# Kernel optimization log

Hardware: AMD Instinct MI355X
Metric: run time of the kernel (lower is better)

Reference implementation:

```python
import jax, jax.numpy as jnp
import numpy as np
from jax import lax

B, S, D = 2, 4096, 1024
E, H, K = 8, 2816, 2  # hidden_dim 4096 -> int(2*4096/3)=2730 -> round up to multiple_of 256 -> 2816


def setup_inputs() -> dict:
    key = jax.random.key(0)
    ks = jax.random.split(key, 5)
    scale = 0.02
    return {
        "x": jax.random.normal(ks[0], (B, S, D), dtype=jnp.float32),
        "router_w": jax.random.normal(ks[1], (E, D), dtype=jnp.float32) * scale,
        "w1": jax.random.normal(ks[2], (E, D, H), dtype=jnp.float32) * scale,
        "w2": jax.random.normal(ks[3], (E, H, D), dtype=jnp.float32) * scale,
        "w3": jax.random.normal(ks[4], (E, D, H), dtype=jnp.float32) * scale,
        "top_k": K,
    }


def reference(x, router_w, w1, w2, w3, top_k):
    b, s, d = x.shape
    e = router_w.shape[0]
    xf = x.reshape(-1, d)                                # [T, D]
    logits = xf @ router_w.T                             # [T, E]
    vals, idx = lax.top_k(logits, top_k)                 # [T, K]
    rw = jax.nn.softmax(vals.astype(jnp.float32), axis=-1).astype(x.dtype)  # [T, K]
    # combine[t, e] = routing weight of expert e for token t (0 if not selected)
    combine = jnp.sum(jax.nn.one_hot(idx, e, dtype=x.dtype) * rw[..., None], axis=1)  # [T, E]

    def body(acc, ew):
        w1e, w2e, w3e, ce = ew                           # [D,H], [H,D], [D,H], [T]
        h = jax.nn.silu(xf @ w1e) * (xf @ w3e)           # SwiGLU FFN, [T, H]
        return acc + (h @ w2e) * ce[:, None], None

    out, _ = lax.scan(body, jnp.zeros_like(xf), (w1, w2, w3, combine.T))
    return out.reshape(b, s, d)
```

## Files before the change

### kernel.cpp

```cpp
#include <hip/hip_runtime.h>
#include <stdint.h>

#define T_TOK 8192
#define DIM   1024
#define NE    8
#define NH    2816
#define NROWS (T_TOK*2)

typedef __attribute__((ext_vector_type(8))) __bf16 bf16x8;
typedef __attribute__((ext_vector_type(4))) float  f32x4;

typedef __attribute__((address_space(1))) const unsigned int g_as1;
typedef __attribute__((address_space(3))) unsigned int l_as3;
#define GLL(g, l) __builtin_amdgcn_global_load_lds((g_as1*)(g), (l_as3*)(l), 16, 0, 0)

__device__ __forceinline__ unsigned short f2bf(float f){
  union { float f; uint32_t u; } v; v.f = f;
  uint32_t r = (v.u + 0x7FFFu + ((v.u >> 16) & 1u)) >> 16;
  return (unsigned short)r;
}


__global__ void init_k(int* counts, int* cursor){
  int i = threadIdx.x;
  if (i < NE){ counts[i] = 0; cursor[i] = 0; }
}

__global__ void zero_out_k(float4* __restrict__ out){
  int i = blockIdx.x*blockDim.x + threadIdx.x;
  const int n4 = T_TOK*DIM/4;
  const float4 z = make_float4(0.f,0.f,0.f,0.f);
  for (; i < n4; i += gridDim.x*blockDim.x) out[i] = z;
}

__global__ void cvt_k(const float* __restrict__ x, unsigned short* __restrict__ xbf){
  int i = blockIdx.x*blockDim.x + threadIdx.x;
  const int total = T_TOK*DIM/8;
  for (; i < total; i += gridDim.x*blockDim.x){
    const float4 a = *(const float4*)(x + (size_t)i*8);
    const float4 b = *(const float4*)(x + (size_t)i*8 + 4);
    ushort4 lo = make_ushort4(f2bf(a.x), f2bf(a.y), f2bf(a.z), f2bf(a.w));
    ushort4 hi = make_ushort4(f2bf(b.x), f2bf(b.y), f2bf(b.z), f2bf(b.w));
    *(ushort4*)(xbf + (size_t)i*8)     = lo;
    *(ushort4*)(xbf + (size_t)i*8 + 4) = hi;
  }
}

__global__ __launch_bounds__(256) void transp_k(const float* __restrict__ in,
    unsigned short* __restrict__ outp, int R, int C)
{
  __shared__ unsigned short Tl[64*68];
  const int r0 = blockIdx.x*64, c0 = blockIdx.y*64;
  const size_t mbase = (size_t)blockIdx.z * (size_t)R * (size_t)C;
  const float* ip = in + mbase;
  unsigned short* op = outp + mbase;
  const int t = threadIdx.x;
  #pragma unroll
  for (int i=0;i<4;i++){
    const int r  = (t>>4) + i*16;
    const int cq = t & 15;
    const float4 v = *(const float4*)(ip + (size_t)(r0+r)*C + c0 + cq*4);
    Tl[(cq*4+0)*68 + r] = f2bf(v.x);
    Tl[(cq*4+1)*68 + r] = f2bf(v.y);
    Tl[(cq*4+2)*68 + r] = f2bf(v.z);
    Tl[(cq*4+3)*68 + r] = f2bf(v.w);
  }
  __syncthreads();
  #pragma unroll
  for (int i=0;i<4;i++){
    const int idx = i*1024 + t*4;
    const int c = idx>>6, r = idx&63;
    const ushort4 v = *(const ushort4*)&Tl[c*68 + r];
    *(ushort4*)(op + (size_t)(c0+c)*R + r0 + r) = v;
  }
}

__global__ __launch_bounds__(256) void transp2_k(const float* __restrict__ w1,
    const float* __restrict__ w3, unsigned short* __restrict__ w1t,
    unsigned short* __restrict__ w3t)
{
  __shared__ unsigned short Tl[64*68];
  const int r0 = blockIdx.x*64, c0 = blockIdx.y*64;
  const int z = blockIdx.z;
  const size_t mbase = (size_t)(z & (NE-1)) * (size_t)DIM * (size_t)NH;
  const float* ip = (z < NE ? w1 : w3) + mbase;
  unsigned short* op = (z < NE ? w1t : w3t) + mbase;
  const int t = threadIdx.x;
  #pragma unroll
  for (int i=0;i<4;i++){
    const int r  = (t>>4) + i*16;
    const int cq = t & 15;
    const float4 v = *(const float4*)(ip + (size_t)(r0+r)*NH + c0 + cq*4);
    Tl[(cq*4+0)*68 + r] = f2bf(v.x);
    Tl[(cq*4+1)*68 + r] = f2bf(v.y);
    Tl[(cq*4+2)*68 + r] = f2bf(v.z);
    Tl[(cq*4+3)*68 + r] = f2bf(v.w);
  }
  __syncthreads();
  #pragma unroll
  for (int i=0;i<4;i++){
    const int idx = i*1024 + t*4;
    const int c = idx>>6, r = idx&63;
    const ushort4 v = *(const ushort4*)&Tl[c*68 + r];
    *(ushort4*)(op + (size_t)(c0+c)*DIM + r0 + r) = v;
  }
}


__global__ void router_k(const float* __restrict__ x, const float* __restrict__ rw,
                         int* __restrict__ topk_e, float* __restrict__ topk_w,
                         int* __restrict__ counts){
  const int t = blockIdx.x;
  const int l = threadIdx.x;
  const float* xr = x + (size_t)t * DIM;
  float acc[NE];
  #pragma unroll
  for (int e=0;e<NE;e++) acc[e] = 0.f;
  #pragma unroll
  for (int i=0;i<DIM/64;i++){
    float xv = xr[l + 64*i];
    #pragma unroll
    for (int e=0;e<NE;e++) acc[e] += xv * rw[e*DIM + l + 64*i];
  }
  #pragma unroll
  for (int e=0;e<NE;e++){
    float v = acc[e];
    #pragma unroll
    for (int off=32; off; off>>=1) v += __shfl_xor(v, off);
    acc[e] = v;
  }
  if (l == 0){
    int e0 = 0; float v0 = acc[0];
    #pragma unroll
    for (int e=1;e<NE;e++) if (acc[e] > v0){ v0 = acc[e]; e0 = e; }
    int e1 = -1; float v1 = -1e30f;
    #pragma unroll
    for (int e=0;e<NE;e++) if (e != e0 && acc[e] > v1){ v1 = acc[e]; e1 = e; }
    float ex = __expf(v1 - v0);
    float s  = 1.f + ex;
    topk_e[t*2]   = e0;  topk_e[t*2+1] = e1;
    topk_w[t*2]   = 1.f/s; topk_w[t*2+1] = ex/s;
    atomicAdd(&counts[e0], 1);
    atomicAdd(&counts[e1], 1);
  }
}

__global__ void prefix_k(const int* __restrict__ counts, int* __restrict__ offs){
  if (threadIdx.x == 0 && blockIdx.x == 0){
    int s = 0;
    for (int e=0;e<NE;e++){ offs[e] = s; s += counts[e]; }
  }
}

__global__ void scatter_k(const int* __restrict__ topk_e, const float* __restrict__ topk_w,
                          const int* __restrict__ offs, int* __restrict__ cursor,
                          int* __restrict__ row_tok, float* __restrict__ row_w){
  int t = blockIdx.x*blockDim.x + threadIdx.x;
  if (t >= T_TOK) return;
  #pragma unroll
  for (int k=0;k<2;k++){
    int e = topk_e[t*2+k];
    int p = atomicAdd(&cursor[e], 1);
    int flat = offs[e] + p;
    row_tok[flat] = t;
    row_w[flat]   = topk_w[t*2+k];
  }
}


__global__ __launch_bounds__(512,2) void gemm1_bf(
    const unsigned short* __restrict__ xbf,
    const unsigned short* __restrict__ w1t, const unsigned short* __restrict__ w3t,
    unsigned short* __restrict__ hbuf,
    const int* __restrict__ row_tok,
    const int* __restrict__ counts, const int* __restrict__ offs)
{
  __shared__ unsigned short Al [2][128*32];
  __shared__ unsigned short B1l[2][128*32];
  __shared__ unsigned short B3l[2][128*32];

  const int i   = blockIdx.y*64 + blockIdx.x;
  const int lid = (i & 7)*1408 + (i >> 3);
  const int e   = lid / 1408;
  const int rem = lid - e*1408;
  const int h0  = (rem >> 6) * 128;
  const int rb  = rem & 63;

  const int cnt = counts[e];
  const int row0 = rb * 128;
  if (row0 >= cnt) return;
  const int nv   = min(128, cnt - row0);
  const int base = offs[e] + row0;

  const int t  = threadIdx.x;
  const int srow = t >> 2, sch = t & 3;
  const int tok = row_tok[base + min(srow, nv-1)];
  const unsigned short* asrc = xbf + (size_t)tok*DIM + sch*8;
  const unsigned short* b1s  = w1t + ((size_t)(e*NH + h0 + srow))*DIM + sch*8;
  const unsigned short* b3s  = w3t + ((size_t)(e*NH + h0 + srow))*DIM + sch*8;
  const int lo = t*16;

  const int wid = t >> 6, l = t & 63;
  const int wr = wid >> 2, wc = wid & 3;
  const int lr = l & 15,  lk = l >> 4;

  f32x4 acc1[4][2], acc3[4][2];
  #pragma unroll
  for (int m=0;m<4;m++)
    #pragma unroll
    for (int n=0;n<2;n++){ acc1[m][n] = (f32x4)0.f; acc3[m][n] = (f32x4)0.f; }

  GLL(asrc, (char*)Al [0] + lo);
  GLL(b1s,  (char*)B1l[0] + lo);
  GLL(b3s,  (char*)B3l[0] + lo);
  __syncthreads();

  for (int kk=0; kk<DIM/32; ++kk){
    const int cur = kk & 1;
    if (kk < DIM/32 - 1){
      const int k1 = (kk+1)*32;
      GLL(asrc + k1, (char*)Al [cur^1] + lo);
      GLL(b1s  + k1, (char*)B1l[cur^1] + lo);
      GLL(b3s  + k1, (char*)B3l[cur^1] + lo);
    }
    bf16x8 a[4], b1[2], b3[2];
    #pragma unroll
    for (int m=0;m<4;m++) a[m] = *(const bf16x8*)&Al[cur][(wr*64 + m*16 + lr)*32 + lk*8];
    #pragma unroll
    for (int n=0;n<2;n++){
      b1[n] = *(const bf16x8*)&B1l[cur][(wc*32 + n*16 + lr)*32 + lk*8];
      b3[n] = *(const bf16x8*)&B3l[cur][(wc*32 + n*16 + lr)*32 + lk*8];
    }
    #pragma unroll
    for (int m=0;m<4;m++)
      #pragma unroll
      for (int n=0;n<2;n++){
        acc1[m][n] = __builtin_amdgcn_mfma_f32_16x16x32_bf16(a[m], b1[n], acc1[m][n], 0,0,0);
        acc3[m][n] = __builtin_amdgcn_mfma_f32_16x16x32_bf16(a[m], b3[n], acc3[m][n], 0,0,0);
      }
    __syncthreads();
  }

  #pragma unroll
  for (int m=0;m<4;m++){
    #pragma unroll
    for (int i2=0;i2<4;i2++){
      const int r = wr*64 + m*16 + lk*4 + i2;
      if (r < nv){
        const size_t rowbase = (size_t)(base + r) * NH;
        #pragma unroll
        for (int n=0;n<2;n++){
          float z  = acc1[m][n][i2];
          float p3 = acc3[m][n][i2];
          float hv = (z / (1.f + __expf(-z))) * p3;
          hbuf[rowbase + h0 + wc*32 + n*16 + lr] = f2bf(hv);
        }
      }
    }
  }
}

__global__ __launch_bounds__(512,2) void gemm2_bf(
    const unsigned short* __restrict__ hbuf,
    const unsigned short* __restrict__ w2t,
    float* __restrict__ out,
    const int* __restrict__ row_tok, const float* __restrict__ row_w,
    const int* __restrict__ counts, const int* __restrict__ offs)
{
  __shared__ unsigned short Al[2][128*32];
  __shared__ unsigned short Bl[2][128*32];

  const int i   = blockIdx.y*64 + blockIdx.x;
  const int lid = (i & 7)*512 + (i >> 3);
  const int e   = lid >> 9;
  const int rem = lid & 511;
  const int d0  = (rem >> 6) * 128;
  const int rb  = rem & 63;

  const int cnt = counts[e];
  const int row0 = rb * 128;
  if (row0 >= cnt) return;
  const int nv   = min(128, cnt - row0);
  const int base = offs[e] + row0;

  const int t  = threadIdx.x;
  const int srow = t >> 2, sch = t & 3;
  const unsigned short* asrc = hbuf + (size_t)(base + min(srow, nv-1))*NH + sch*8;
  const unsigned short* bs   = w2t + ((size_t)(e*DIM + d0 + srow))*NH + sch*8;
  const int lo = t*16;

  const int wid = t >> 6, l = t & 63;
  const int wr = wid >> 2, wc = wid & 3;
  const int lr = l & 15,  lk = l >> 4;

  f32x4 acc[4][2];
  #pragma unroll
  for (int m=0;m<4;m++)
    #pragma unroll
    for (int n=0;n<2;n++) acc[m][n] = (f32x4)0.f;

  GLL(asrc, (char*)Al[0] + lo);
  GLL(bs,   (char*)Bl[0] + lo);
  __syncthreads();

  for (int kk=0; kk<NH/32; ++kk){
    const int cur = kk & 1;
    if (kk < NH/32 - 1){
      const int k1 = (kk+1)*32;
      GLL(asrc + k1, (char*)Al[cur^1] + lo);
      GLL(bs   + k1, (char*)Bl[cur^1] + lo);
    }
    bf16x8 a[4], b[2];
    #pragma unroll
    for (int m=0;m<4;m++) a[m] = *(const bf16x8*)&Al[cur][(wr*64 + m*16 + lr)*32 + lk*8];
    #pragma unroll
    for (int n=0;n<2;n++)  b[n] = *(const bf16x8*)&Bl[cur][(wc*32 + n*16 + lr)*32 + lk*8];
    #pragma unroll
    for (int m=0;m<4;m++)
      #pragma unroll
      for (int n=0;n<2;n++)
        acc[m][n] = __builtin_amdgcn_mfma_f32_16x16x32_bf16(a[m], b[n], acc[m][n], 0,0,0);
    __syncthreads();
  }

  #pragma unroll
  for (int m=0;m<4;m++){
    #pragma unroll
    for (int i2=0;i2<4;i2++){
      const int r = wr*64 + m*16 + lk*4 + i2;
      if (r < nv){
        const int flat = base + r;
        const int tok  = row_tok[flat];
        const float wgt = row_w[flat];
        float* orow = out + (size_t)tok * DIM + d0 + wc*32;
        #pragma unroll
        for (int n=0;n<2;n++)
          atomicAdd(&orow[n*16 + lr], acc[m][n][i2] * wgt);
      }
    }
  }
}


__global__ __launch_bounds__(256) void gemm1_k(
    const unsigned short* __restrict__ xbf,
    const float* __restrict__ w1, const float* __restrict__ w3,
    unsigned short* __restrict__ hbuf,
    const int* __restrict__ row_tok,
    const int* __restrict__ counts, const int* __restrict__ offs)
{
  __shared__ unsigned short Al [128*32];
  __shared__ unsigned short B1l[128*32];
  __shared__ unsigned short B3l[128*32];
  const int e   = blockIdx.y >> 6;
  const int rb  = blockIdx.y & 63;
  const int cnt = counts[e];
  const int row0 = rb * 128;
  if (row0 >= cnt) return;
  const int nv   = min(128, cnt - row0);
  const int base = offs[e] + row0;
  const int h0   = blockIdx.x * 128;
  const int t  = threadIdx.x;
  const int ar0 = t >> 2;
  const int ac  = t & 3;
  const int tok0 = row_tok[base + min(ar0,      nv-1)];
  const int tok1 = row_tok[base + min(ar0 + 64, nv-1)];
  const size_t asrc0 = (size_t)tok0 * DIM + ac*8;
  const size_t asrc1 = (size_t)tok1 * DIM + ac*8;
  const int dg = t >> 5;
  const int hq = t & 31;
  const float* w1p = w1 + (size_t)e * DIM * NH + (size_t)(h0 + hq*4);
  const float* w3p = w3 + (size_t)e * DIM * NH + (size_t)(h0 + hq*4);
  const int wid = t >> 6, l = t & 63;
  const int wr = wid >> 1, wc = wid & 1;
  const int lr = l & 15,  lk = l >> 4;
  f32x4 acc1[4][4], acc3[4][4];
  #pragma unroll
  for (int m=0;m<4;m++)
    #pragma unroll
    for (int n=0;n<4;n++){ acc1[m][n] = (f32x4)0.f; acc3[m][n] = (f32x4)0.f; }
  for (int kk=0; kk<DIM/32; ++kk){
    const int k0 = kk*32;
    __syncthreads();
    *(uint4*)&Al[ar0*32 + ac*8]      = *(const uint4*)(xbf + asrc0 + k0);
    *(uint4*)&Al[(ar0+64)*32 + ac*8] = *(const uint4*)(xbf + asrc1 + k0);
    {
      const float4 f0 = *(const float4*)(w1p + (size_t)(k0 + dg*4 + 0)*NH);
      const float4 f1 = *(const float4*)(w1p + (size_t)(k0 + dg*4 + 1)*NH);
      const float4 f2 = *(const float4*)(w1p + (size_t)(k0 + dg*4 + 2)*NH);
      const float4 f3 = *(const float4*)(w1p + (size_t)(k0 + dg*4 + 3)*NH);
      const float* p0=(const float*)&f0; const float* p1=(const float*)&f1;
      const float* p2=(const float*)&f2; const float* p3=(const float*)&f3;
      #pragma unroll
      for (int j=0;j<4;j++){
        ushort4 pk = make_ushort4(f2bf(p0[j]), f2bf(p1[j]), f2bf(p2[j]), f2bf(p3[j]));
        *(ushort4*)&B1l[(hq*4+j)*32 + dg*4] = pk;
      }
      const float4 g0 = *(const float4*)(w3p + (size_t)(k0 + dg*4 + 0)*NH);
      const float4 g1 = *(const float4*)(w3p + (size_t)(k0 + dg*4 + 1)*NH);
      const float4 g2 = *(const float4*)(w3p + (size_t)(k0 + dg*4 + 2)*NH);
      const float4 g3 = *(const float4*)(w3p + (size_t)(k0 + dg*4 + 3)*NH);
      const float* q0=(const float*)&g0; const float* q1=(const float*)&g1;
      const float* q2=(const float*)&g2; const float* q3=(const float*)&g3;
      #pragma unroll
      for (int j=0;j<4;j++){
        ushort4 pk = make_ushort4(f2bf(q0[j]), f2bf(q1[j]), f2bf(q2[j]), f2bf(q3[j]));
        *(ushort4*)&B3l[(hq*4+j)*32 + dg*4] = pk;
      }
    }
    __syncthreads();
    bf16x8 a[4], b1[4], b3[4];
    #pragma unroll
    for (int m=0;m<4;m++) a[m] = *(const bf16x8*)&Al[(wr*64 + m*16 + lr)*32 + lk*8];
    #pragma unroll
    for (int n=0;n<4;n++){
      b1[n] = *(const bf16x8*)&B1l[(wc*64 + n*16 + lr)*32 + lk*8];
      b3[n] = *(const bf16x8*)&B3l[(wc*64 + n*16 + lr)*32 + lk*8];
    }
    #pragma unroll
    for (int m=0;m<4;m++)
      #pragma unroll
      for (int n=0;n<4;n++){
        acc1[m][n] = __builtin_amdgcn_mfma_f32_16x16x32_bf16(a[m], b1[n], acc1[m][n], 0,0,0);
        acc3[m][n] = __builtin_amdgcn_mfma_f32_16x16x32_bf16(a[m], b3[n], acc3[m][n], 0,0,0);
      }
  }
  #pragma unroll
  for (int m=0;m<4;m++){
    #pragma unroll
    for (int i=0;i<4;i++){
      const int r = wr*64 + m*16 + lk*4 + i;
      if (r < nv){
        const size_t rowbase = (size_t)(base + r) * NH;
        #pragma unroll
        for (int n=0;n<4;n++){
          float z  = acc1[m][n][i];
          float p3 = acc3[m][n][i];
          float hv = (z / (1.f + __expf(-z))) * p3;
          hbuf[rowbase + h0 + wc*64 + n*16 + lr] = f2bf(hv);
        }
      }
    }
  }
}

__global__ __launch_bounds__(256) void gemm2_k(
    const unsigned short* __restrict__ hbuf,
    const float* __restrict__ w2,
    float* __restrict__ out,
    const int* __restrict__ row_tok, const float* __restrict__ row_w,
    const int* __restrict__ counts, const int* __restrict__ offs)
{
  __shared__ unsigned short Al[128*32];
  __shared__ unsigned short Bl[128*32];
  const int e   = blockIdx.y >> 6;
  const int rb  = blockIdx.y & 63;
  const int cnt = counts[e];
  const int row0 = rb * 128;
  if (row0 >= cnt) return;
  const int nv   = min(128, cnt - row0);
  const int base = offs[e] + row0;
  const int d0   = blockIdx.x * 128;
  const int t  = threadIdx.x;
  const int ar0 = t >> 2;
  const int ac  = t & 3;
  const size_t asrc0 = (size_t)(base + min(ar0,      nv-1)) * NH + ac*8;
  const size_t asrc1 = (size_t)(base + min(ar0 + 64, nv-1)) * NH + ac*8;
  const int dg = t >> 5;
  const int hq = t & 31;
  const float* w2p = w2 + (size_t)e * NH * DIM + (size_t)(d0 + hq*4);
  const int wid = t >> 6, l = t & 63;
  const int wr = wid >> 1, wc = wid & 1;
  const int lr = l & 15,  lk = l >> 4;
  f32x4 acc[4][4];
  #pragma unroll
  for (int m=0;m<4;m++)
    #pragma unroll
    for (int n=0;n<4;n++) acc[m][n] = (f32x4)0.f;
  for (int kk=0; kk<NH/32; ++kk){
    const int k0 = kk*32;
    __syncthreads();
    *(uint4*)&Al[ar0*32 + ac*8]      = *(const uint4*)(hbuf + asrc0 + k0);
    *(uint4*)&Al[(ar0+64)*32 + ac*8] = *(const uint4*)(hbuf + asrc1 + k0);
    {
      const float4 f0 = *(const float4*)(w2p + (size_t)(k0 + dg*4 + 0)*DIM);
      const float4 f1 = *(const float4*)(w2p + (size_t)(k0 + dg*4 + 1)*DIM);
      const float4 f2 = *(const float4*)(w2p + (size_t)(k0 + dg*4 + 2)*DIM);
      const float4 f3 = *(const float4*)(w2p + (size_t)(k0 + dg*4 + 3)*DIM);
      const float* p0=(const float*)&f0; const float* p1=(const float*)&f1;
      const float* p2=(const float*)&f2; const float* p3=(const float*)&f3;
      #pragma unroll
      for (int j=0;j<4;j++){
        ushort4 pk = make_ushort4(f2bf(p0[j]), f2bf(p1[j]), f2bf(p2[j]), f2bf(p3[j]));
        *(ushort4*)&Bl[(hq*4+j)*32 + dg*4] = pk;
      }
    }
    __syncthreads();
    bf16x8 a[4], b[4];
    #pragma unroll
    for (int m=0;m<4;m++) a[m] = *(const bf16x8*)&Al[(wr*64 + m*16 + lr)*32 + lk*8];
    #pragma unroll
    for (int n=0;n<4;n++)  b[n] = *(const bf16x8*)&Bl[(wc*64 + n*16 + lr)*32 + lk*8];
    #pragma unroll
    for (int m=0;m<4;m++)
      #pragma unroll
      for (int n=0;n<4;n++)
        acc[m][n] = __builtin_amdgcn_mfma_f32_16x16x32_bf16(a[m], b[n], acc[m][n], 0,0,0);
  }
  #pragma unroll
  for (int m=0;m<4;m++){
    #pragma unroll
    for (int i=0;i<4;i++){
      const int r = wr*64 + m*16 + lk*4 + i;
      if (r < nv){
        const int flat = base + r;
        const int tok  = row_tok[flat];
        const float wgt = row_w[flat];
        float* orow = out + (size_t)tok * DIM + d0 + wc*64;
        #pragma unroll
        for (int n=0;n<4;n++)
          atomicAdd(&orow[n*16 + lr], acc[m][n][i] * wgt);
      }
    }
  }
}


extern "C" void kernel_launch(void* const* d_in, const int* in_sizes, int n_in,
                              void* d_out, int out_size, void* d_ws, size_t ws_size,
                              hipStream_t stream) {
  (void)in_sizes; (void)n_in; (void)out_size;
  const float* x   = (const float*)d_in[0];
  const float* rw  = (const float*)d_in[1];
  const float* w1  = (const float*)d_in[2];
  const float* w2  = (const float*)d_in[3];
  const float* w3  = (const float*)d_in[4];
  float* out = (float*)d_out;
  char* ws = (char*)d_ws;

  const size_t SZ_XBF  = (size_t)T_TOK*DIM*2;
  const size_t SZ_HBUF = (size_t)NROWS*NH*2;
  const size_t SZ_WT   = (size_t)NE*NH*DIM*2;
  const size_t SZ_SMALL = (size_t)NROWS*4*2 + (size_t)T_TOK*2*4*2 + 3*64*4 + 4096;
  const size_t NEED_FAST = SZ_XBF + SZ_HBUF + 2*SZ_WT + SZ_SMALL;

  if (ws_size >= NEED_FAST) {
    size_t off = 0;
    unsigned short* xbf  = (unsigned short*)(ws + off); off += SZ_XBF;
    unsigned short* hbuf = (unsigned short*)(ws + off); off += SZ_HBUF;
    unsigned short* w1t  = (unsigned short*)(ws + off); off += SZ_WT;
    unsigned short* w3t  = (unsigned short*)(ws + off); off += SZ_WT;
    unsigned short* w2t  = w1t;
    int*   row_tok = (int*)  (ws + off); off += NROWS*4;
    float* row_w   = (float*)(ws + off); off += NROWS*4;
    int*   topk_e  = (int*)  (ws + off); off += T_TOK*2*4;
    float* topk_w  = (float*)(ws + off); off += T_TOK*2*4;
    int*   counts  = (int*)  (ws + off); off += 64;
    int*   offs    = (int*)  (ws + off); off += 64;
    int*   cursor  = (int*)  (ws + off); off += 64;

    init_k    <<<1, 64, 0, stream>>>(counts, cursor);
    zero_out_k<<<2048, 256, 0, stream>>>((float4*)out);
    cvt_k     <<<2048, 256, 0, stream>>>(x, xbf);
    router_k  <<<T_TOK, 64, 0, stream>>>(x, rw, topk_e, topk_w, counts);
    prefix_k  <<<1, 64, 0, stream>>>(counts, offs);
    scatter_k <<<(T_TOK+255)/256, 256, 0, stream>>>(topk_e, topk_w, offs, cursor, row_tok, row_w);
    transp2_k <<<dim3(DIM/64, NH/64, 2*NE), 256, 0, stream>>>(w1, w3, w1t, w3t);
    gemm1_bf  <<<dim3(64, NE*22), 512, 0, stream>>>(xbf, w1t, w3t, hbuf, row_tok, counts, offs);
    transp_k  <<<dim3(NH/64, DIM/64, NE), 256, 0, stream>>>(w2, w2t, NH, DIM);
    gemm2_bf  <<<dim3(64, NE*8), 512, 0, stream>>>(hbuf, w2t, out, row_tok, row_w, counts, offs);
  } else {
    size_t off = 0;
    unsigned short* xbf  = (unsigned short*)(ws + off); off += SZ_XBF;
    unsigned short* hbuf = (unsigned short*)(ws + off); off += SZ_HBUF;
    int*   row_tok = (int*)  (ws + off); off += NROWS*4;
    float* row_w   = (float*)(ws + off); off += NROWS*4;
    int*   topk_e  = (int*)  (ws + off); off += T_TOK*2*4;
    float* topk_w  = (float*)(ws + off); off += T_TOK*2*4;
    int*   counts  = (int*)  (ws + off); off += 64;
    int*   offs    = (int*)  (ws + off); off += 64;
    int*   cursor  = (int*)  (ws + off); off += 64;

    init_k    <<<1, 64, 0, stream>>>(counts, cursor);
    zero_out_k<<<2048, 256, 0, stream>>>((float4*)out);
    cvt_k     <<<2048, 256, 0, stream>>>(x, xbf);
    router_k  <<<T_TOK, 64, 0, stream>>>(x, rw, topk_e, topk_w, counts);
    prefix_k  <<<1, 64, 0, stream>>>(counts, offs);
    scatter_k <<<(T_TOK+255)/256, 256, 0, stream>>>(topk_e, topk_w, offs, cursor, row_tok, row_w);
    gemm1_k   <<<dim3(NH/128, NE*64), 256, 0, stream>>>(xbf, w1, w3, hbuf, row_tok, counts, offs);
    gemm2_k   <<<dim3(DIM/128, NE*64), 256, 0, stream>>>(hbuf, w2, out, row_tok, row_w, counts, offs);
  }
}
```

Before: 770.8 us.

## Triple-buffer expert GEMM LDS pipeline with XOR swizzle and single barrier

Both expert GEMM kernels move from a double-buffered LDS scheme with two __syncthreads per k-step to a three-stage ring. Loads are issued two tiles ahead, and each step waits on an explicit vmcnt before a single s_barrier. Global-to-LDS chunk placement and the matching fragment reads are XOR-swizzled by row to cut LDS bank conflicts. s_setprio is raised around the MFMA block. This should hide more global-load latency and reduce stalls, at the cost of more LDS per block (72KB for gemm1), which could limit occupancy.

```diff
diff --git a/kernel.cpp b/kernel.cpp
--- a/kernel.cpp
+++ b/kernel.cpp
@@ -168,16 +168,16 @@
 }
 
 
-__global__ __launch_bounds__(512,2) void gemm1_bf(
+__global__ __launch_bounds__(512,2) void gemm1_p(
     const unsigned short* __restrict__ xbf,
     const unsigned short* __restrict__ w1t, const unsigned short* __restrict__ w3t,
     unsigned short* __restrict__ hbuf,
     const int* __restrict__ row_tok,
     const int* __restrict__ counts, const int* __restrict__ offs)
 {
-  __shared__ unsigned short Al [2][128*32];
-  __shared__ unsigned short B1l[2][128*32];
-  __shared__ unsigned short B3l[2][128*32];
+  __shared__ unsigned short As [3][128*32];
+  __shared__ unsigned short B1s[3][128*32];
+  __shared__ unsigned short B3s[3][128*32];
 
   const int i   = blockIdx.y*64 + blockIdx.x;
   const int lid = (i & 7)*1408 + (i >> 3);
@@ -191,18 +191,21 @@
   if (row0 >= cnt) return;
   const int nv   = min(128, cnt - row0);
   const int base = offs[e] + row0;
-
-  const int t  = threadIdx.x;
-  const int srow = t >> 2, sch = t & 3;
-  const int tok = row_tok[base + min(srow, nv-1)];
-  const unsigned short* asrc = xbf + (size_t)tok*DIM + sch*8;
-  const unsigned short* b1s  = w1t + ((size_t)(e*NH + h0 + srow))*DIM + sch*8;
-  const unsigned short* b3s  = w3t + ((size_t)(e*NH + h0 + srow))*DIM + sch*8;
+  const int NK   = DIM/32;
+
+  const int t = threadIdx.x;
+  const int r_loc = t >> 2, sct = t & 3;
+  const int csw = (sct ^ ((r_loc >> 1) & 3)) * 8;
+  const int tok = row_tok[base + min(r_loc, nv-1)];
+  const unsigned short* aS  = xbf + (size_t)tok*DIM + csw;
+  const unsigned short* b1S = w1t + ((size_t)(e*NH + h0) + r_loc)*DIM + csw;
+  const unsigned short* b3S = w3t + ((size_t)(e*NH + h0) + r_loc)*DIM + csw;
   const int lo = t*16;
 
   const int wid = t >> 6, l = t & 63;
   const int wr = wid >> 2, wc = wid & 3;
   const int lr = l & 15,  lk = l >> 4;
+  const int rc = (lk ^ ((lr >> 1) & 3)) * 8;
 
   f32x4 acc1[4][2], acc3[4][2];
   #pragma unroll
@@ -210,27 +213,35 @@
     #pragma unroll
     for (int n=0;n<2;n++){ acc1[m][n] = (f32x4)0.f; acc3[m][n] = (f32x4)0.f; }
 
-  GLL(asrc, (char*)Al [0] + lo);
-  GLL(b1s,  (char*)B1l[0] + lo);
-  GLL(b3s,  (char*)B3l[0] + lo);
-  __syncthreads();
-
-  for (int kk=0; kk<DIM/32; ++kk){
-    const int cur = kk & 1;
-    if (kk < DIM/32 - 1){
-      const int k1 = (kk+1)*32;
-      GLL(asrc + k1, (char*)Al [cur^1] + lo);
-      GLL(b1s  + k1, (char*)B1l[cur^1] + lo);
-      GLL(b3s  + k1, (char*)B3l[cur^1] + lo);
-    }
+  GLL(aS,      (char*)As[0]+lo); GLL(b1S,      (char*)B1s[0]+lo); GLL(b3S,      (char*)B3s[0]+lo);
+  GLL(aS+32,   (char*)As[1]+lo); GLL(b1S+32,   (char*)B1s[1]+lo); GLL(b3S+32,   (char*)B3s[1]+lo);
+
+  for (int kt=0; kt<NK; ++kt){
+    if (kt < NK-1) asm volatile("s_waitcnt vmcnt(3)" ::: "memory");
+    else           asm volatile("s_waitcnt vmcnt(0)" ::: "memory");
+    __builtin_amdgcn_s_barrier();
+
+    if (kt+2 < NK){
+      const int kA = (kt+2)*32;
+      char* ad  = (char*)As [(kt+2)%3];
+      char* b1d = (char*)B1s[(kt+2)%3];
+      char* b3d = (char*)B3s[(kt+2)%3];
+      GLL(aS+kA, ad+lo); GLL(b1S+kA, b1d+lo); GLL(b3S+kA, b3d+lo);
+    }
+
+    const unsigned short* Ab  = As [kt%3];
+    const unsigned short* B1b = B1s[kt%3];
+    const unsigned short* B3b = B3s[kt%3];
+
     bf16x8 a[4], b1[2], b3[2];
     #pragma unroll
-    for (int m=0;m<4;m++) a[m] = *(const bf16x8*)&Al[cur][(wr*64 + m*16 + lr)*32 + lk*8];
+    for (int m=0;m<4;m++) a[m] = *(const bf16x8*)&Ab[(wr*64 + m*16 + lr)*32 + rc];
     #pragma unroll
     for (int n=0;n<2;n++){
-      b1[n] = *(const bf16x8*)&B1l[cur][(wc*32 + n*16 + lr)*32 + lk*8];
-      b3[n] = *(const bf16x8*)&B3l[cur][(wc*32 + n*16 + lr)*32 + lk*8];
-    }
+      b1[n] = *(const bf16x8*)&B1b[(wc*32 + n*16 + lr)*32 + rc];
+      b3[n] = *(const bf16x8*)&B3b[(wc*32 + n*16 + lr)*32 + rc];
+    }
+    __builtin_amdgcn_s_setprio(1);
     #pragma unroll
     for (int m=0;m<4;m++)
       #pragma unroll
@@ -238,7 +249,7 @@
         acc1[m][n] = __builtin_amdgcn_mfma_f32_16x16x32_bf16(a[m], b1[n], acc1[m][n], 0,0,0);
         acc3[m][n] = __builtin_amdgcn_mfma_f32_16x16x32_bf16(a[m], b3[n], acc3[m][n], 0,0,0);
       }
-    __syncthreads();
+    __builtin_amdgcn_s_setprio(0);
   }
 
   #pragma unroll
@@ -260,15 +271,15 @@
   }
 }
 
-__global__ __launch_bounds__(512,2) void gemm2_bf(
+__global__ __launch_bounds__(512,2) void gemm2_p(
     const unsigned short* __restrict__ hbuf,
     const unsigned short* __restrict__ w2t,
     float* __restrict__ out,
     const int* __restrict__ row_tok, const float* __restrict__ row_w,
     const int* __restrict__ counts, const int* __restrict__ offs)
 {
-  __shared__ unsigned short Al[2][128*32];
-  __shared__ unsigned short Bl[2][128*32];
+  __shared__ unsigned short As[3][128*32];
+  __shared__ unsigned short Bs[3][128*32];
 
   const int i   = blockIdx.y*64 + blockIdx.x;
   const int lid = (i & 7)*512 + (i >> 3);
@@ -282,16 +293,19 @@
   if (row0 >= cnt) return;
   const int nv   = min(128, cnt - row0);
   const int base = offs[e] + row0;
-
-  const int t  = threadIdx.x;
-  const int srow = t >> 2, sch = t & 3;
-  const unsigned short* asrc = hbuf + (size_t)(base + min(srow, nv-1))*NH + sch*8;
-  const unsigned short* bs   = w2t + ((size_t)(e*DIM + d0 + srow))*NH + sch*8;
+  const int NK   = NH/32;
+
+  const int t = threadIdx.x;
+  const int r_loc = t >> 2, sct = t & 3;
+  const int csw = (sct ^ ((r_loc >> 1) & 3)) * 8;
+  const unsigned short* aS = hbuf + (size_t)(base + min(r_loc, nv-1))*NH + csw;
+  const unsigned short* bS = w2t + ((size_t)(e*DIM + d0) + r_loc)*NH + csw;
   const int lo = t*16;
 
   const int wid = t >> 6, l = t & 63;
   const int wr = wid >> 2, wc = wid & 3;
   const int lr = l & 15,  lk = l >> 4;
+  const int rc = (lk ^ ((lr >> 1) & 3)) * 8;
 
   f32x4 acc[4][2];
   #pragma unroll
@@ -299,28 +313,36 @@
     #pragma unroll
     for (int n=0;n<2;n++) acc[m][n] = (f32x4)0.f;
 
-  GLL(asrc, (char*)Al[0] + lo);
-  GLL(bs,   (char*)Bl[0] + lo);
-  __syncthreads();
-
-  for (int kk=0; kk<NH/32; ++kk){
-    const int cur = kk & 1;
-    if (kk < NH/32 - 1){
-      const int k1 = (kk+1)*32;
-      GLL(asrc + k1, (char*)Al[cur^1] + lo);
-      GLL(bs   + k1, (char*)Bl[cur^1] + lo);
-    }
+  GLL(aS,    (char*)As[0]+lo); GLL(bS,    (char*)Bs[0]+lo);
+  GLL(aS+32, (char*)As[1]+lo); GLL(bS+32, (char*)Bs[1]+lo);
+
+  for (int kt=0; kt<NK; ++kt){
+    if (kt < NK-1) asm volatile("s_waitcnt vmcnt(2)" ::: "memory");
+    else           asm volatile("s_waitcnt vmcnt(0)" ::: "memory");
+    __builtin_amdgcn_s_barrier();
+
+    if (kt+2 < NK){
+      const int kA = (kt+2)*32;
+      char* ad = (char*)As[(kt+2)%3];
+      char* bd = (char*)Bs[(kt+2)%3];
+      GLL(aS+kA, ad+lo); GLL(bS+kA, bd+lo);
+    }
+
+    const unsigned short* Ab = As[kt%3];
+    const unsigned short* Bb = Bs[kt%3];
+
     bf16x8 a[4], b[2];
     #pragma unroll
-    for (int m=0;m<4;m++) a[m] = *(const bf16x8*)&Al[cur][(wr*64 + m*16 + lr)*32 + lk*8];
-    #pragma unroll
-    for (int n=0;n<2;n++)  b[n] = *(const bf16x8*)&Bl[cur][(wc*32 + n*16 + lr)*32 + lk*8];
+    for (int m=0;m<4;m++) a[m] = *(const bf16x8*)&Ab[(wr*64 + m*16 + lr)*32 + rc];
+    #pragma unroll
+    for (int n=0;n<2;n++)  b[n] = *(const bf16x8*)&Bb[(wc*32 + n*16 + lr)*32 + rc];
+    __builtin_amdgcn_s_setprio(1);
     #pragma unroll
     for (int m=0;m<4;m++)
       #pragma unroll
       for (int n=0;n<2;n++)
         acc[m][n] = __builtin_amdgcn_mfma_f32_16x16x32_bf16(a[m], b[n], acc[m][n], 0,0,0);
-    __syncthreads();
+    __builtin_amdgcn_s_setprio(0);
   }
 
   #pragma unroll
@@ -566,9 +588,9 @@
     prefix_k  <<<1, 64, 0, stream>>>(counts, offs);
     scatter_k <<<(T_TOK+255)/256, 256, 0, stream>>>(topk_e, topk_w, offs, cursor, row_tok, row_w);
     transp2_k <<<dim3(DIM/64, NH/64, 2*NE), 256, 0, stream>>>(w1, w3, w1t, w3t);
-    gemm1_bf  <<<dim3(64, NE*22), 512, 0, stream>>>(xbf, w1t, w3t, hbuf, row_tok, counts, offs);
+    gemm1_p   <<<dim3(64, NE*22), 512, 0, stream>>>(xbf, w1t, w3t, hbuf, row_tok, counts, offs);
     transp_k  <<<dim3(NH/64, DIM/64, NE), 256, 0, stream>>>(w2, w2t, NH, DIM);
-    gemm2_bf  <<<dim3(64, NE*8), 512, 0, stream>>>(hbuf, w2t, out, row_tok, row_w, counts, offs);
+    gemm2_p   <<<dim3(64, NE*8), 512, 0, stream>>>(hbuf, w2t, out, row_tok, row_w, counts, offs);
   } else {
     size_t off = 0;
     unsigned short* xbf  = (unsigned short*)(ws + off); off += SZ_XBF;
```

After: 755.9 us. About the same (-1.9%).

## Enlarge MoE GEMM tiles to 256 rows with swizzled LDS and phased pipeline

Applied to the files above, without the earlier changes.

Both expert GEMMs now use 256-row token tiles with K-steps of 64, and gemm2 also widens to 256 output columns. LDS uses an XOR swizzle to avoid bank conflicts, and the next tile's global-to-LDS loads are split across four compute phases with explicit vmcnt waits, barriers and setprio around MFMA bursts. The aim is more data reuse per loaded byte and better overlap of loads with matrix math. In exchange, register and LDS use rise and there are fewer blocks, which can hurt occupancy and tail balance across experts with uneven token counts.

```diff
diff --git a/kernel.cpp b/kernel.cpp
--- a/kernel.cpp
+++ b/kernel.cpp
@@ -13,6 +13,7 @@
 typedef __attribute__((address_space(1))) const unsigned int g_as1;
 typedef __attribute__((address_space(3))) unsigned int l_as3;
 #define GLL(g, l) __builtin_amdgcn_global_load_lds((g_as1*)(g), (l_as3*)(l), 16, 0, 0)
+#define MFMA16(a,b,c) __builtin_amdgcn_mfma_f32_16x16x32_bf16(a,b,c,0,0,0)
 
 __device__ __forceinline__ unsigned short f2bf(float f){
   union { float f; uint32_t u; } v; v.f = f;
@@ -168,16 +169,16 @@
 }
 
 
-__global__ __launch_bounds__(512,2) void gemm1_bf(
+__global__ __launch_bounds__(512,2) void gemm1_8p(
     const unsigned short* __restrict__ xbf,
     const unsigned short* __restrict__ w1t, const unsigned short* __restrict__ w3t,
     unsigned short* __restrict__ hbuf,
     const int* __restrict__ row_tok,
     const int* __restrict__ counts, const int* __restrict__ offs)
 {
-  __shared__ unsigned short Al [2][128*32];
-  __shared__ unsigned short B1l[2][128*32];
-  __shared__ unsigned short B3l[2][128*32];
+  __shared__ unsigned short As [2][256*64];
+  __shared__ unsigned short B1s[2][128*64];
+  __shared__ unsigned short B3s[2][128*64];
 
   const int i   = blockIdx.y*64 + blockIdx.x;
   const int lid = (i & 7)*1408 + (i >> 3);
@@ -186,66 +187,115 @@
   const int h0  = (rem >> 6) * 128;
   const int rb  = rem & 63;
 
-  const int cnt = counts[e];
-  const int row0 = rb * 128;
+  const int cnt  = counts[e];
+  const int row0 = rb * 256;
   if (row0 >= cnt) return;
-  const int nv   = min(128, cnt - row0);
+  const int nv   = min(256, cnt - row0);
   const int base = offs[e] + row0;
+  const int NK   = DIM/64;
 
   const int t  = threadIdx.x;
-  const int srow = t >> 2, sch = t & 3;
-  const int tok = row_tok[base + min(srow, nv-1)];
-  const unsigned short* asrc = xbf + (size_t)tok*DIM + sch*8;
-  const unsigned short* b1s  = w1t + ((size_t)(e*NH + h0 + srow))*DIM + sch*8;
-  const unsigned short* b3s  = w3t + ((size_t)(e*NH + h0 + srow))*DIM + sch*8;
+  const int r8 = t >> 3, sl = t & 7;
+  const int csw = ((sl ^ (r8 & 7)) << 3);
+  const int tk0 = row_tok[base + min(r8,       nv-1)];
+  const int tk1 = row_tok[base + min(r8 + 64,  nv-1)];
+  const int tk2 = row_tok[base + min(r8 + 128, nv-1)];
+  const int tk3 = row_tok[base + min(r8 + 192, nv-1)];
+  const unsigned short* aP0 = xbf + (size_t)tk0*DIM + csw;
+  const unsigned short* aP1 = xbf + (size_t)tk1*DIM + csw;
+  const unsigned short* aP2 = xbf + (size_t)tk2*DIM + csw;
+  const unsigned short* aP3 = xbf + (size_t)tk3*DIM + csw;
+  const unsigned short* b1P0 = w1t + ((size_t)(e*NH + h0) + r8)*DIM + csw;
+  const unsigned short* b1P1 = b1P0 + (size_t)64*DIM;
+  const unsigned short* b3P0 = w3t + ((size_t)(e*NH + h0) + r8)*DIM + csw;
+  const unsigned short* b3P1 = b3P0 + (size_t)64*DIM;
   const int lo = t*16;
 
   const int wid = t >> 6, l = t & 63;
   const int wr = wid >> 2, wc = wid & 3;
   const int lr = l & 15,  lk = l >> 4;
 
-  f32x4 acc1[4][2], acc3[4][2];
-  #pragma unroll
-  for (int m=0;m<4;m++)
+  f32x4 acc1[8][2], acc3[8][2];
+  #pragma unroll
+  for (int m=0;m<8;m++)
     #pragma unroll
     for (int n=0;n<2;n++){ acc1[m][n] = (f32x4)0.f; acc3[m][n] = (f32x4)0.f; }
 
-  GLL(asrc, (char*)Al [0] + lo);
-  GLL(b1s,  (char*)B1l[0] + lo);
-  GLL(b3s,  (char*)B3l[0] + lo);
-  __syncthreads();
-
-  for (int kk=0; kk<DIM/32; ++kk){
-    const int cur = kk & 1;
-    if (kk < DIM/32 - 1){
-      const int k1 = (kk+1)*32;
-      GLL(asrc + k1, (char*)Al [cur^1] + lo);
-      GLL(b1s  + k1, (char*)B1l[cur^1] + lo);
-      GLL(b3s  + k1, (char*)B3l[cur^1] + lo);
-    }
-    bf16x8 a[4], b1[2], b3[2];
-    #pragma unroll
-    for (int m=0;m<4;m++) a[m] = *(const bf16x8*)&Al[cur][(wr*64 + m*16 + lr)*32 + lk*8];
-    #pragma unroll
-    for (int n=0;n<2;n++){
-      b1[n] = *(const bf16x8*)&B1l[cur][(wc*32 + n*16 + lr)*32 + lk*8];
-      b3[n] = *(const bf16x8*)&B3l[cur][(wc*32 + n*16 + lr)*32 + lk*8];
-    }
-    #pragma unroll
-    for (int m=0;m<4;m++)
-      #pragma unroll
-      for (int n=0;n<2;n++){
-        acc1[m][n] = __builtin_amdgcn_mfma_f32_16x16x32_bf16(a[m], b1[n], acc1[m][n], 0,0,0);
-        acc3[m][n] = __builtin_amdgcn_mfma_f32_16x16x32_bf16(a[m], b3[n], acc3[m][n], 0,0,0);
-      }
-    __syncthreads();
-  }
-
-  #pragma unroll
-  for (int m=0;m<4;m++){
+  GLL(b1P0, (char*)B1s[0] + lo);          GLL(b1P1, (char*)B1s[0] + 8192 + lo);
+  GLL(b3P0, (char*)B3s[0] + lo);          GLL(b3P1, (char*)B3s[0] + 8192 + lo);
+  GLL(aP0,  (char*)As[0]  + lo);          GLL(aP2,  (char*)As[0]  + 16384 + lo);
+  GLL(aP1,  (char*)As[0]  + 8192 + lo);   GLL(aP3,  (char*)As[0]  + 24576 + lo);
+  asm volatile("s_waitcnt vmcnt(2)" ::: "memory");
+  __builtin_amdgcn_s_barrier();
+
+  for (int kt=0; kt<NK; ++kt){
+    const int cur = kt & 1;
+    const int kof = (kt+1)*64;
+    const unsigned short* Ab  = As [cur];
+    const unsigned short* B1b = B1s[cur];
+    const unsigned short* B3b = B3s[cur];
+    char* Ad  = (char*)As [cur^1];
+    char* B1d = (char*)B1s[cur^1];
+    char* B3d = (char*)B3s[cur^1];
+    const bool st = (kt+1 < NK);
+
+    bf16x8 b1f[2][2], b3f[2][2];
+    #pragma unroll
+    for (int p=0; p<4; ++p){
+      bf16x8 a[2][2];
+      #pragma unroll
+      for (int j=0;j<2;j++){
+        const int row = wr*128 + (p*2+j)*16 + lr;
+        #pragma unroll
+        for (int ks=0;ks<2;ks++){
+          const int ck = ks*4 + lk;
+          a[j][ks] = *(const bf16x8*)&Ab[row*64 + ((ck ^ (row & 7)) << 3)];
+        }
+      }
+      if (p==0){
+        #pragma unroll
+        for (int n=0;n<2;n++){
+          const int brow = wc*32 + n*16 + lr;
+          #pragma unroll
+          for (int ks=0;ks<2;ks++){
+            const int ck = ks*4 + lk;
+            const int boff = brow*64 + ((ck ^ (brow & 7)) << 3);
+            b1f[n][ks] = *(const bf16x8*)&B1b[boff];
+            b3f[n][ks] = *(const bf16x8*)&B3b[boff];
+          }
+        }
+      }
+      if (st){
+        if      (p==0){ GLL(b1P0+kof, B1d+lo);      GLL(b1P1+kof, B1d+8192+lo); }
+        else if (p==1){ GLL(b3P0+kof, B3d+lo);      GLL(b3P1+kof, B3d+8192+lo); }
+        else if (p==2){ GLL(aP0+kof,  Ad+lo);       GLL(aP2+kof,  Ad+16384+lo); }
+        else          { GLL(aP1+kof,  Ad+8192+lo);  GLL(aP3+kof,  Ad+24576+lo); }
+      }
+      if (p==1){ if (st) asm volatile("s_waitcnt vmcnt(4)" ::: "memory");
+                 else    asm volatile("s_waitcnt vmcnt(0)" ::: "memory"); }
+      if (p==3){ asm volatile("s_waitcnt vmcnt(2)" ::: "memory"); }
+      __builtin_amdgcn_s_barrier();
+      asm volatile("s_waitcnt lgkmcnt(0)" ::: "memory");
+      __builtin_amdgcn_s_setprio(1);
+      #pragma unroll
+      for (int j=0;j<2;j++)
+        #pragma unroll
+        for (int ks=0;ks<2;ks++)
+          #pragma unroll
+          for (int n=0;n<2;n++){
+            acc1[p*2+j][n] = MFMA16(a[j][ks], b1f[n][ks], acc1[p*2+j][n]);
+            acc3[p*2+j][n] = MFMA16(a[j][ks], b3f[n][ks], acc3[p*2+j][n]);
+          }
+      __builtin_amdgcn_s_setprio(0);
+      __builtin_amdgcn_s_barrier();
+    }
+  }
+
+  #pragma unroll
+  for (int m=0;m<8;m++){
     #pragma unroll
     for (int i2=0;i2<4;i2++){
-      const int r = wr*64 + m*16 + lk*4 + i2;
+      const int r = wr*128 + m*16 + lk*4 + i2;
       if (r < nv){
         const size_t rowbase = (size_t)(base + r) * NH;
         #pragma unroll
@@ -260,81 +310,129 @@
   }
 }
 
-__global__ __launch_bounds__(512,2) void gemm2_bf(
+__global__ __launch_bounds__(512,2) void gemm2_8p(
     const unsigned short* __restrict__ hbuf,
     const unsigned short* __restrict__ w2t,
     float* __restrict__ out,
     const int* __restrict__ row_tok, const float* __restrict__ row_w,
     const int* __restrict__ counts, const int* __restrict__ offs)
 {
-  __shared__ unsigned short Al[2][128*32];
-  __shared__ unsigned short Bl[2][128*32];
+  __shared__ unsigned short As[2][256*64];
+  __shared__ unsigned short Bs[2][256*64];
 
   const int i   = blockIdx.y*64 + blockIdx.x;
-  const int lid = (i & 7)*512 + (i >> 3);
-  const int e   = lid >> 9;
-  const int rem = lid & 511;
-  const int d0  = (rem >> 6) * 128;
+  const int lid = (i & 7)*256 + (i >> 3);
+  const int e   = lid >> 8;
+  const int rem = lid & 255;
+  const int d0  = (rem >> 6) * 256;
   const int rb  = rem & 63;
 
-  const int cnt = counts[e];
-  const int row0 = rb * 128;
+  const int cnt  = counts[e];
+  const int row0 = rb * 256;
   if (row0 >= cnt) return;
-  const int nv   = min(128, cnt - row0);
+  const int nv   = min(256, cnt - row0);
   const int base = offs[e] + row0;
+  const int NK   = NH/64;
 
   const int t  = threadIdx.x;
-  const int srow = t >> 2, sch = t & 3;
-  const unsigned short* asrc = hbuf + (size_t)(base + min(srow, nv-1))*NH + sch*8;
-  const unsigned short* bs   = w2t + ((size_t)(e*DIM + d0 + srow))*NH + sch*8;
+  const int r8 = t >> 3, sl = t & 7;
+  const int csw = ((sl ^ (r8 & 7)) << 3);
+  const unsigned short* aP0 = hbuf + (size_t)(base + min(r8,       nv-1))*NH + csw;
+  const unsigned short* aP1 = hbuf + (size_t)(base + min(r8 + 64,  nv-1))*NH + csw;
+  const unsigned short* aP2 = hbuf + (size_t)(base + min(r8 + 128, nv-1))*NH + csw;
+  const unsigned short* aP3 = hbuf + (size_t)(base + min(r8 + 192, nv-1))*NH + csw;
+  const unsigned short* bP0 = w2t + ((size_t)(e*DIM + d0) + r8)*NH + csw;
+  const unsigned short* bP1 = bP0 + (size_t)64*NH;
+  const unsigned short* bP2 = bP0 + (size_t)128*NH;
+  const unsigned short* bP3 = bP0 + (size_t)192*NH;
   const int lo = t*16;
 
   const int wid = t >> 6, l = t & 63;
   const int wr = wid >> 2, wc = wid & 3;
   const int lr = l & 15,  lk = l >> 4;
 
-  f32x4 acc[4][2];
-  #pragma unroll
-  for (int m=0;m<4;m++)
-    #pragma unroll
-    for (int n=0;n<2;n++) acc[m][n] = (f32x4)0.f;
-
-  GLL(asrc, (char*)Al[0] + lo);
-  GLL(bs,   (char*)Bl[0] + lo);
-  __syncthreads();
-
-  for (int kk=0; kk<NH/32; ++kk){
-    const int cur = kk & 1;
-    if (kk < NH/32 - 1){
-      const int k1 = (kk+1)*32;
-      GLL(asrc + k1, (char*)Al[cur^1] + lo);
-      GLL(bs   + k1, (char*)Bl[cur^1] + lo);
-    }
-    bf16x8 a[4], b[2];
-    #pragma unroll
-    for (int m=0;m<4;m++) a[m] = *(const bf16x8*)&Al[cur][(wr*64 + m*16 + lr)*32 + lk*8];
-    #pragma unroll
-    for (int n=0;n<2;n++)  b[n] = *(const bf16x8*)&Bl[cur][(wc*32 + n*16 + lr)*32 + lk*8];
-    #pragma unroll
-    for (int m=0;m<4;m++)
-      #pragma unroll
-      for (int n=0;n<2;n++)
-        acc[m][n] = __builtin_amdgcn_mfma_f32_16x16x32_bf16(a[m], b[n], acc[m][n], 0,0,0);
-    __syncthreads();
-  }
-
-  #pragma unroll
-  for (int m=0;m<4;m++){
+  f32x4 acc[8][4];
+  #pragma unroll
+  for (int m=0;m<8;m++)
+    #pragma unroll
+    for (int n=0;n<4;n++) acc[m][n] = (f32x4)0.f;
+
+  GLL(bP0, (char*)Bs[0] + lo);          GLL(bP1, (char*)Bs[0] + 8192 + lo);
+  GLL(bP2, (char*)Bs[0] + 16384 + lo);  GLL(bP3, (char*)Bs[0] + 24576 + lo);
+  GLL(aP0, (char*)As[0] + lo);          GLL(aP2, (char*)As[0] + 16384 + lo);
+  GLL(aP1, (char*)As[0] + 8192 + lo);   GLL(aP3, (char*)As[0] + 24576 + lo);
+  asm volatile("s_waitcnt vmcnt(2)" ::: "memory");
+  __builtin_amdgcn_s_barrier();
+
+  for (int kt=0; kt<NK; ++kt){
+    const int cur = kt & 1;
+    const int kof = (kt+1)*64;
+    const unsigned short* Ab = As[cur];
+    const unsigned short* Bb = Bs[cur];
+    char* Ad = (char*)As[cur^1];
+    char* Bd = (char*)Bs[cur^1];
+    const bool st = (kt+1 < NK);
+
+    bf16x8 bf[4][2];
+    #pragma unroll
+    for (int p=0; p<4; ++p){
+      bf16x8 a[2][2];
+      #pragma unroll
+      for (int j=0;j<2;j++){
+        const int row = wr*128 + (p*2+j)*16 + lr;
+        #pragma unroll
+        for (int ks=0;ks<2;ks++){
+          const int ck = ks*4 + lk;
+          a[j][ks] = *(const bf16x8*)&Ab[row*64 + ((ck ^ (row & 7)) << 3)];
+        }
+      }
+      if (p==0){
+        #pragma unroll
+        for (int n=0;n<4;n++){
+          const int brow = wc*64 + n*16 + lr;
+          #pragma unroll
+          for (int ks=0;ks<2;ks++){
+            const int ck = ks*4 + lk;
+            bf[n][ks] = *(const bf16x8*)&Bb[brow*64 + ((ck ^ (brow & 7)) << 3)];
+          }
+        }
+      }
+      if (st){
+        if      (p==0){ GLL(bP0+kof, Bd+lo);        GLL(bP1+kof, Bd+8192+lo); }
+        else if (p==1){ GLL(bP2+kof, Bd+16384+lo);  GLL(bP3+kof, Bd+24576+lo); }
+        else if (p==2){ GLL(aP0+kof, Ad+lo);        GLL(aP2+kof, Ad+16384+lo); }
+        else          { GLL(aP1+kof, Ad+8192+lo);   GLL(aP3+kof, Ad+24576+lo); }
+      }
+      if (p==1){ if (st) asm volatile("s_waitcnt vmcnt(4)" ::: "memory");
+                 else    asm volatile("s_waitcnt vmcnt(0)" ::: "memory"); }
+      if (p==3){ asm volatile("s_waitcnt vmcnt(2)" ::: "memory"); }
+      __builtin_amdgcn_s_barrier();
+      asm volatile("s_waitcnt lgkmcnt(0)" ::: "memory");
+      __builtin_amdgcn_s_setprio(1);
+      #pragma unroll
+      for (int j=0;j<2;j++)
+        #pragma unroll
+        for (int ks=0;ks<2;ks++)
+          #pragma unroll
+          for (int n=0;n<4;n++)
+            acc[p*2+j][n] = MFMA16(a[j][ks], bf[n][ks], acc[p*2+j][n]);
+      __builtin_amdgcn_s_setprio(0);
+      __builtin_amdgcn_s_barrier();
+    }
+  }
+
+  #pragma unroll
+  for (int m=0;m<8;m++){
     #pragma unroll
     for (int i2=0;i2<4;i2++){
-      const int r = wr*64 + m*16 + lk*4 + i2;
+      const int r = wr*128 + m*16 + lk*4 + i2;
       if (r < nv){
         const int flat = base + r;
         const int tok  = row_tok[flat];
         const float wgt = row_w[flat];
-        float* orow = out + (size_t)tok * DIM + d0 + wc*32;
-        #pragma unroll
-        for (int n=0;n<2;n++)
+        float* orow = out + (size_t)tok * DIM + d0 + wc*64;
+        #pragma unroll
+        for (int n=0;n<4;n++)
           atomicAdd(&orow[n*16 + lr], acc[m][n][i2] * wgt);
       }
     }
@@ -421,8 +519,8 @@
     for (int m=0;m<4;m++)
       #pragma unroll
       for (int n=0;n<4;n++){
-        acc1[m][n] = __builtin_amdgcn_mfma_f32_16x16x32_bf16(a[m], b1[n], acc1[m][n], 0,0,0);
-        acc3[m][n] = __builtin_amdgcn_mfma_f32_16x16x32_bf16(a[m], b3[n], acc3[m][n], 0,0,0);
+        acc1[m][n] = MFMA16(a[m], b1[n], acc1[m][n]);
+        acc3[m][n] = MFMA16(a[m], b3[n], acc3[m][n]);
       }
   }
   #pragma unroll
@@ -505,7 +603,7 @@
     for (int m=0;m<4;m++)
       #pragma unroll
       for (int n=0;n<4;n++)
-        acc[m][n] = __builtin_amdgcn_mfma_f32_16x16x32_bf16(a[m], b[n], acc[m][n], 0,0,0);
+        acc[m][n] = MFMA16(a[m], b[n], acc[m][n]);
   }
   #pragma unroll
   for (int m=0;m<4;m++){
@@ -566,9 +664,9 @@
     prefix_k  <<<1, 64, 0, stream>>>(counts, offs);
     scatter_k <<<(T_TOK+255)/256, 256, 0, stream>>>(topk_e, topk_w, offs, cursor, row_tok, row_w);
     transp2_k <<<dim3(DIM/64, NH/64, 2*NE), 256, 0, stream>>>(w1, w3, w1t, w3t);
-    gemm1_bf  <<<dim3(64, NE*22), 512, 0, stream>>>(xbf, w1t, w3t, hbuf, row_tok, counts, offs);
+    gemm1_8p  <<<dim3(64, 176), 512, 0, stream>>>(xbf, w1t, w3t, hbuf, row_tok, counts, offs);
     transp_k  <<<dim3(NH/64, DIM/64, NE), 256, 0, stream>>>(w2, w2t, NH, DIM);
-    gemm2_bf  <<<dim3(64, NE*8), 512, 0, stream>>>(hbuf, w2t, out, row_tok, row_w, counts, offs);
+    gemm2_8p  <<<dim3(64, 32), 512, 0, stream>>>(hbuf, w2t, out, row_tok, row_w, counts, offs);
   } else {
     size_t off = 0;
     unsigned short* xbf  = (unsigned short*)(ws + off); off += SZ_XBF;
```

Measured after the change: 877.1 us. 1.14x slower.
